# Kernel optimization log

Measured on AMD Instinct MI355X. Metric: run time of the kernel, lower is better.

Reference implementation:

```python
import jax, jax.numpy as jnp
import numpy as np

N, K, D, H, HD = 65536, 16, 96, 384, 256
DEPTH = 4

def _gelu(x):
    # torch nn.GELU default is exact erf-based
    return jax.nn.gelu(x, approximate=False)

def _bn(t, g, b):
    # eval-mode BatchNorm1d with running_mean=0, running_var=1 -> affine
    return t * g + b

def _mlp(f, w1, b1, w2, g, b):
    # Mlp: Linear(D,H)+GELU+Linear(H,D,no bias)+BN
    return _bn(_gelu(f @ w1 + b1) @ w2, g, b)


def setup_inputs() -> dict:
    key = jax.random.key(0)
    ks = jax.random.split(key, 32)
    def w(i, shape, s=0.05):
        return (jax.random.normal(ks[i], shape) * s).astype(jnp.float32)
    def g(i, shape):
        return (1.0 + 0.1 * jax.random.normal(ks[i], shape)).astype(jnp.float32)
    return dict(
        x=jax.random.normal(ks[0], (N, 4), jnp.float32),
        xyz=jax.random.uniform(ks[1], (N, 3), jnp.float32),
        knn=jax.random.randint(ks[2], (N, K), 0, N, dtype=jnp.int32),
        ne_w1=w(3, (7, 16)), ne_g1=g(4, (16,)), ne_b1=w(5, (16,)),
        ne_w2=w(6, (16, 32)), ne_g2=g(7, (32,)), ne_b2=w(8, (32,)),
        ne_w3=w(9, (32, D)),
        nbr_g=g(10, (D,)), nbr_b=w(11, (D,)),
        m0_w1=w(12, (D, H)), m0_b1=w(13, (H,)), m0_w2=w(14, (H, D)),
        m0_g=g(15, (D,)), m0_b=w(16, (D,)),
        lfp_w=w(17, (DEPTH, D, D)), lfp_g=g(18, (DEPTH, D)), lfp_b=w(19, (DEPTH, D)),
        ms_w1=w(20, (DEPTH // 2, D, H)), ms_b1=w(21, (DEPTH // 2, H)),
        ms_w2=w(22, (DEPTH // 2, H, D)), ms_g=g(23, (DEPTH // 2, D)), ms_b=w(24, (DEPTH // 2, D)),
        pp_g=g(25, (D,)), pp_b=w(26, (D,)), pp_w=w(27, (D, HD)),
    )


def reference(x, xyz, knn, ne_w1, ne_g1, ne_b1, ne_w2, ne_g2, ne_b2, ne_w3,
              nbr_g, nbr_b, m0_w1, m0_b1, m0_w2, m0_g, m0_b,
              lfp_w, lfp_g, lfp_b, ms_w1, ms_b1, ms_w2, ms_g, ms_b,
              pp_g, pp_b, pp_w):
    # --- neighbor embedding (first stage): rel-xyz + gathered raw features ---
    rel = xyz[knn] - xyz[:, None, :]               # [N,K,3]
    nbr = jnp.concatenate([rel, x[knn]], axis=-1)  # [N,K,7]
    h = _gelu(_bn(nbr @ ne_w1, ne_g1, ne_b1))      # [N,K,16]
    h = _gelu(_bn(h @ ne_w2, ne_g2, ne_b2))        # [N,K,32]
    h = h @ ne_w3                                  # [N,K,D]
    f = _bn(jnp.max(h, axis=1), nbr_g, nbr_b)      # edge max-pool -> [N,D]

    # --- Block: mlp + DEPTH x (LFP [+ Mlp every 2nd]) with residuals ---
    f = f + _mlp(f, m0_w1, m0_b1, m0_w2, m0_g, m0_b)
    for i in range(DEPTH):
        y = f @ lfp_w[i]                                       # proj [N,D]
        y = _bn(jnp.max(y[knn], axis=1) - y, lfp_g[i], lfp_b[i])  # knn edge maxpool
        f = f + y
        if i % 2 == 1:
            j = i // 2
            f = f + _mlp(f, ms_w1[j], ms_b1[j], ms_w2[j], ms_g[j], ms_b[j])

    # --- post projection head ---
    return _bn(f, pp_g, pp_b) @ pp_w               # [N,HD]
```

## Files before the change

kernel.cpp:

```cpp
#include <hip/hip_runtime.h>
#include <hip/hip_bf16.h>
#include <math.h>

#define NPTS 65536
#define KNB  16

typedef __attribute__((ext_vector_type(8))) short bf16x8;
typedef __attribute__((ext_vector_type(4))) float f32x4;

__device__ __forceinline__ float gelu_f(float v) {
    const float z  = v * 0.70710678118654752f;
    const float az = fabsf(z);
    const float t  = __builtin_amdgcn_rcpf(fmaf(0.3275911f, az, 1.0f));
    float p = fmaf(t, 1.061405429f, -1.453152027f);
    p = fmaf(t, p, 1.421413741f);
    p = fmaf(t, p, -0.284496736f);
    p = fmaf(t, p, 0.254829592f);
    p = p * t;
    const float e  = __expf(-z * z);
    float er = fmaf(-p, e, 1.0f);
    er = copysignf(er, z);
    return 0.5f * v * (1.0f + er);
}

__device__ __forceinline__ short f2bf_s(float v) {
    __hip_bfloat16 h = __float2bfloat16(v);
    return *reinterpret_cast<short*>(&h);
}

__global__ __launch_bounds__(256) void prep_weights(
    const float* __restrict__ m0_w1, const float* __restrict__ m0_w2,
    const float* __restrict__ ms_w1, const float* __restrict__ ms_w2,
    const float* __restrict__ lfp_w,
    const float* __restrict__ pp_w, const float* __restrict__ pp_g,
    const float* __restrict__ pp_b,
    __hip_bfloat16* __restrict__ w_m0w1t, __hip_bfloat16* __restrict__ w_m0w2t,
    __hip_bfloat16* __restrict__ w_msw1t, __hip_bfloat16* __restrict__ w_msw2t,
    __hip_bfloat16* __restrict__ w_lfpt,  __hip_bfloat16* __restrict__ w_ppt,
    float* __restrict__ c_pp)
{
    int idx = blockIdx.x * 256 + threadIdx.x;
    if (idx < 36864) {
        int n = idx / 96, k = idx % 96;
        w_m0w1t[idx] = __float2bfloat16(m0_w1[k * 384 + n]);
        return;
    }
    idx -= 36864;
    if (idx < 36864) {
        int n = idx / 384, k = idx % 384;
        w_m0w2t[idx] = __float2bfloat16(m0_w2[k * 96 + n]);
        return;
    }
    idx -= 36864;
    if (idx < 2 * 36864) {
        int j = idx / 36864, r = idx % 36864;
        int n = r / 96, k = r % 96;
        w_msw1t[idx] = __float2bfloat16(ms_w1[j * 36864 + k * 384 + n]);
        return;
    }
    idx -= 2 * 36864;
    if (idx < 2 * 36864) {
        int j = idx / 36864, r = idx % 36864;
        int n = r / 384, k = r % 384;
        w_msw2t[idx] = __float2bfloat16(ms_w2[j * 36864 + k * 96 + n]);
        return;
    }
    idx -= 2 * 36864;
    if (idx < 4 * 9216) {
        int i = idx / 9216, r = idx % 9216;
        int n = r / 96, k = r % 96;
        w_lfpt[idx] = __float2bfloat16(lfp_w[i * 9216 + k * 96 + n]);
        return;
    }
    idx -= 4 * 9216;
    if (idx < 24576) {
        int n = idx / 96, k = idx % 96;
        w_ppt[idx] = __float2bfloat16(pp_g[k] * pp_w[k * 256 + n]);
        return;
    }
    idx -= 24576;
    if (idx < 256) {
        float s = 0.f;
        for (int k = 0; k < 96; ++k) s += pp_b[k] * pp_w[k * 256 + idx];
        c_pp[idx] = s;
    }
}

__global__ __launch_bounds__(256) void ne_kernel(
    const float* __restrict__ x, const float* __restrict__ xyz,
    const int* __restrict__ knn,
    const float* __restrict__ w1, const float* __restrict__ g1, const float* __restrict__ b1,
    const float* __restrict__ w2, const float* __restrict__ g2, const float* __restrict__ b2,
    const float* __restrict__ w3,
    const float* __restrict__ ng, const float* __restrict__ nb,
    float* __restrict__ f, __hip_bfloat16* __restrict__ fbf)
{
    __shared__ float w1s[7 * 16];
    __shared__ float g1s[16], b1s[16], g2s[32], b2s[32];
    __shared__ float ngs[96], nbs[96];
    __shared__ short h16s[256][24];
    __shared__ short w2ts[32][40];
    __shared__ short h32s[256][40];
    __shared__ short w3t[96][40];

    const int tid = threadIdx.x;
    for (int i = tid; i < 112; i += 256) w1s[i] = w1[i];
    for (int i = tid; i < 1280; i += 256) {
        const int o = i / 40, kk = i % 40;
        w2ts[o][kk] = (kk < 16) ? f2bf_s(w2[kk * 32 + o]) : (short)0;
    }
    if (tid < 16) { g1s[tid] = g1[tid]; b1s[tid] = b1[tid]; }
    if (tid < 32) { g2s[tid] = g2[tid]; b2s[tid] = b2[tid]; }
    if (tid < 96) { ngs[tid] = ng[tid]; nbs[tid] = nb[tid]; }
    for (int i = tid; i < 3072; i += 256) {
        const int c = i / 96, n = i % 96;
        w3t[n][c] = f2bf_s(w3[i]);
    }
    __syncthreads();

    const int pl = tid >> 4;
    const int k  = tid & 15;
    const int p  = blockIdx.x * 16 + pl;
    const int j  = knn[p * KNB + k];

    float in7[7];
    {
        float cx0 = xyz[p * 3 + 0], cx1 = xyz[p * 3 + 1], cx2 = xyz[p * 3 + 2];
        in7[0] = xyz[j * 3 + 0] - cx0;
        in7[1] = xyz[j * 3 + 1] - cx1;
        in7[2] = xyz[j * 3 + 2] - cx2;
        in7[3] = x[j * 4 + 0];
        in7[4] = x[j * 4 + 1];
        in7[5] = x[j * 4 + 2];
        in7[6] = x[j * 4 + 3];
    }

    {
        bf16x8 t0, t1;
#pragma unroll
        for (int o = 0; o < 16; ++o) {
            float s = 0.f;
#pragma unroll
            for (int c = 0; c < 7; ++c) s += in7[c] * w1s[c * 16 + o];
            const float hv = gelu_f(s * g1s[o] + b1s[o]);
            if (o < 8) t0[o] = f2bf_s(hv); else t1[o - 8] = f2bf_s(hv);
        }
        *(bf16x8*)&h16s[tid][0] = t0;
        *(bf16x8*)&h16s[tid][8] = t1;
    }
    __syncthreads();

    const int wave = tid >> 6;
    const int lane = tid & 63;
    const int lr   = lane & 15;
    const int kc   = (lane >> 4) * 8;
    const f32x4 zero = {0.f, 0.f, 0.f, 0.f};
    const bf16x8 zero8 = {0, 0, 0, 0, 0, 0, 0, 0};

    {
        const float g2r0 = g2s[lr],      b2r0 = b2s[lr];
        const float g2r1 = g2s[16 + lr], b2r1 = b2s[16 + lr];
        const bf16x8 w2v0 = *(const bf16x8*)&w2ts[lr][kc];
        const bf16x8 w2v1 = *(const bf16x8*)&w2ts[16 + lr][kc];
#pragma unroll
        for (int pp = 0; pp < 4; ++pp) {
            const int lpl = wave * 4 + pp;
            bf16x8 av = zero8;
            if (lane < 32) av = *(const bf16x8*)&h16s[lpl * 16 + lr][kc];
            f32x4 c0 = __builtin_amdgcn_mfma_f32_16x16x32_bf16(av, w2v0, zero, 0, 0, 0);
            f32x4 c1 = __builtin_amdgcn_mfma_f32_16x16x32_bf16(av, w2v1, zero, 0, 0, 0);
#pragma unroll
            for (int r = 0; r < 4; ++r) {
                const int erow = lpl * 16 + (lane >> 4) * 4 + r;
                h32s[erow][lr]      = f2bf_s(gelu_f(fmaf(c0[r], g2r0, b2r0)));
                h32s[erow][16 + lr] = f2bf_s(gelu_f(fmaf(c1[r], g2r1, b2r1)));
            }
        }
    }
    __syncthreads();

    bf16x8 bv[6];
#pragma unroll
    for (int ct = 0; ct < 6; ++ct)
        bv[ct] = *(const bf16x8*)&w3t[ct * 16 + lr][kc];

#pragma unroll
    for (int pp = 0; pp < 4; ++pp) {
        const int lpl = wave * 4 + pp;
        const int gp  = blockIdx.x * 16 + lpl;
        const bf16x8 av = *(const bf16x8*)&h32s[lpl * 16 + lr][kc];
#pragma unroll
        for (int ct = 0; ct < 6; ++ct) {
            f32x4 a = __builtin_amdgcn_mfma_f32_16x16x32_bf16(av, bv[ct], zero, 0, 0, 0);
            float m = fmaxf(fmaxf(a[0], a[1]), fmaxf(a[2], a[3]));
            m = fmaxf(m, __shfl_xor(m, 16));
            m = fmaxf(m, __shfl_xor(m, 32));
            if (lane < 16) {
                const int d = ct * 16 + lane;
                const float val = m * ngs[d] + nbs[d];
                f[(size_t)gp * 96 + d] = val;
                fbf[(size_t)gp * 96 + d] = __float2bfloat16(val);
            }
        }
    }
}

__global__ __launch_bounds__(256) void mlp_fused(
    const __hip_bfloat16* __restrict__ w1t, const float* __restrict__ b1,
    const __hip_bfloat16* __restrict__ w2t,
    const float* __restrict__ g, const float* __restrict__ b,
    float* __restrict__ f, __hip_bfloat16* __restrict__ fbf)
{
    __shared__ short As[64 * 104];
    __shared__ short Hs[64 * 72];
    __shared__ short Bs[6912];
    __shared__ float bias_s[384];
    __shared__ float gs[96], bs[96];

    const int tid  = threadIdx.x;
    const int wave = tid >> 6;
    const int lane = tid & 63;
    const int lr   = lane & 15;
    const int kc   = (lane >> 4) * 8;
    const int row0 = blockIdx.x * 64;

    const short* fb = (const short*)fbf;
    const short* w1 = (const short*)w1t;
    const short* w2 = (const short*)w2t;

    {
        const int sr = tid >> 2, sk = (tid & 3) * 8;
#pragma unroll
        for (int i = 0; i < 3; ++i)
            *(bf16x8*)&As[sr * 104 + sk + 32 * i] =
                *(const bf16x8*)&fb[(size_t)(row0 + sr) * 96 + sk + 32 * i];
        for (int i = tid; i < 384; i += 256) bias_s[i] = b1[i];
        if (tid < 96) { gs[tid] = g[tid]; bs[tid] = b[tid]; }
    }

    f32x4 acc2[6];
#pragma unroll
    for (int i = 0; i < 6; ++i) acc2[i] = f32x4{0.f, 0.f, 0.f, 0.f};

    for (int c = 0; c < 6; ++c) {
        __syncthreads();
        {
            const int sr = tid >> 2, sk = (tid & 3) * 8;
#pragma unroll
            for (int i = 0; i < 3; ++i)
                *(bf16x8*)&Bs[sr * 104 + sk + 32 * i] =
                    *(const bf16x8*)&w1[(size_t)(c * 64 + sr) * 96 + sk + 32 * i];
        }
        __syncthreads();

        {
            f32x4 acc1[4];
#pragma unroll
            for (int i = 0; i < 4; ++i) acc1[i] = f32x4{0.f, 0.f, 0.f, 0.f};
#pragma unroll
            for (int k0 = 0; k0 < 96; k0 += 32) {
                const bf16x8 av = *(const bf16x8*)&As[(wave * 16 + lr) * 104 + k0 + kc];
#pragma unroll
                for (int ct = 0; ct < 4; ++ct) {
                    const bf16x8 bv = *(const bf16x8*)&Bs[(ct * 16 + lr) * 104 + k0 + kc];
                    acc1[ct] = __builtin_amdgcn_mfma_f32_16x16x32_bf16(av, bv, acc1[ct], 0, 0, 0);
                }
            }
            const int er = wave * 16 + ((lane >> 4) << 2);
#pragma unroll
            for (int ct = 0; ct < 4; ++ct) {
                const int cl = ct * 16 + lr;
                const float bb1 = bias_s[c * 64 + cl];
#pragma unroll
                for (int r = 0; r < 4; ++r)
                    Hs[(er + r) * 72 + cl] = f2bf_s(gelu_f(acc1[ct][r] + bb1));
            }
        }
        __syncthreads();

        {
            for (int i = tid; i < 768; i += 256) {
                const int r = i >> 3, ko = (i & 7) * 8;
                *(bf16x8*)&Bs[r * 72 + ko] =
                    *(const bf16x8*)&w2[(size_t)r * 384 + c * 64 + ko];
            }
        }
        __syncthreads();

#pragma unroll
        for (int ks = 0; ks < 64; ks += 32) {
            const bf16x8 av = *(const bf16x8*)&Hs[(wave * 16 + lr) * 72 + ks + kc];
#pragma unroll
            for (int ct = 0; ct < 6; ++ct) {
                const bf16x8 bv = *(const bf16x8*)&Bs[(ct * 16 + lr) * 72 + ks + kc];
                acc2[ct] = __builtin_amdgcn_mfma_f32_16x16x32_bf16(av, bv, acc2[ct], 0, 0, 0);
            }
        }
    }

    const int er = wave * 16 + ((lane >> 4) << 2);
#pragma unroll
    for (int ct = 0; ct < 6; ++ct) {
        const int col = ct * 16 + lr;
        const float gg = gs[col], bb = bs[col];
#pragma unroll
        for (int r = 0; r < 4; ++r) {
            const size_t o = (size_t)(row0 + er + r) * 96 + col;
            const float nf = f[o] + acc2[ct][r] * gg + bb;
            f[o] = nf;
            fbf[o] = __float2bfloat16(nf);
        }
    }
}

__global__ __launch_bounds__(256) void proj_kernel(
    const __hip_bfloat16* __restrict__ fbf,
    const __hip_bfloat16* __restrict__ wT,
    float* __restrict__ y)
{
    __shared__ short As[64 * 104];
    __shared__ short Ws[96 * 104];

    const int tid  = threadIdx.x;
    const int wave = tid >> 6;
    const int lane = tid & 63;
    const int lr   = lane & 15;
    const int kc   = (lane >> 4) * 8;
    const int row0 = blockIdx.x * 64;

    const short* fb = (const short*)fbf;
    const short* wg = (const short*)wT;

    {
        const int sr = tid >> 2, sk = (tid & 3) * 8;
#pragma unroll
        for (int i = 0; i < 3; ++i)
            *(bf16x8*)&As[sr * 104 + sk + 32 * i] =
                *(const bf16x8*)&fb[(size_t)(row0 + sr) * 96 + sk + 32 * i];
        for (int i = tid; i < 1152; i += 256) {
            const int r = i / 12, ko = (i % 12) * 8;
            *(bf16x8*)&Ws[r * 104 + ko] = *(const bf16x8*)&wg[(size_t)r * 96 + ko];
        }
    }
    __syncthreads();

    f32x4 acc[6];
#pragma unroll
    for (int i = 0; i < 6; ++i) acc[i] = f32x4{0.f, 0.f, 0.f, 0.f};

#pragma unroll
    for (int k0 = 0; k0 < 96; k0 += 32) {
        const bf16x8 av = *(const bf16x8*)&As[(wave * 16 + lr) * 104 + k0 + kc];
#pragma unroll
        for (int ct = 0; ct < 6; ++ct) {
            const bf16x8 bv = *(const bf16x8*)&Ws[(ct * 16 + lr) * 104 + k0 + kc];
            acc[ct] = __builtin_amdgcn_mfma_f32_16x16x32_bf16(av, bv, acc[ct], 0, 0, 0);
        }
    }

    const int er = wave * 16 + ((lane >> 4) << 2);
#pragma unroll
    for (int ct = 0; ct < 6; ++ct) {
        const int col = ct * 16 + lr;
#pragma unroll
        for (int r = 0; r < 4; ++r)
            y[(size_t)(row0 + er + r) * 96 + col] = acc[ct][r];
    }
}

__global__ __launch_bounds__(256) void head_kernel(
    const __hip_bfloat16* __restrict__ fbf,
    const __hip_bfloat16* __restrict__ wT,
    const float* __restrict__ c_pp,
    float* __restrict__ out)
{
    __shared__ short As[64 * 104];
    __shared__ short Bs[64 * 104];
    __shared__ float cpps[256];

    const int tid  = threadIdx.x;
    const int wave = tid >> 6;
    const int lane = tid & 63;
    const int lr   = lane & 15;
    const int kc   = (lane >> 4) * 8;
    const int row0 = blockIdx.x * 64;

    const short* fb = (const short*)fbf;
    const short* wg = (const short*)wT;

    {
        const int sr = tid >> 2, sk = (tid & 3) * 8;
#pragma unroll
        for (int i = 0; i < 3; ++i)
            *(bf16x8*)&As[sr * 104 + sk + 32 * i] =
                *(const bf16x8*)&fb[(size_t)(row0 + sr) * 96 + sk + 32 * i];
        if (tid < 256) cpps[tid] = c_pp[tid];
    }

    for (int nt = 0; nt < 4; ++nt) {
        __syncthreads();
        {
            const int sr = tid >> 2, sk = (tid & 3) * 8;
#pragma unroll
            for (int i = 0; i < 3; ++i)
                *(bf16x8*)&Bs[sr * 104 + sk + 32 * i] =
                    *(const bf16x8*)&wg[(size_t)(nt * 64 + sr) * 96 + sk + 32 * i];
        }
        __syncthreads();

        f32x4 acc[4];
#pragma unroll
        for (int i = 0; i < 4; ++i) acc[i] = f32x4{0.f, 0.f, 0.f, 0.f};
#pragma unroll
        for (int k0 = 0; k0 < 96; k0 += 32) {
            const bf16x8 av = *(const bf16x8*)&As[(wave * 16 + lr) * 104 + k0 + kc];
#pragma unroll
            for (int ct = 0; ct < 4; ++ct) {
                const bf16x8 bv = *(const bf16x8*)&Bs[(ct * 16 + lr) * 104 + k0 + kc];
                acc[ct] = __builtin_amdgcn_mfma_f32_16x16x32_bf16(av, bv, acc[ct], 0, 0, 0);
            }
        }

        const int er = wave * 16 + ((lane >> 4) << 2);
#pragma unroll
        for (int ct = 0; ct < 4; ++ct) {
            const int col = nt * 64 + ct * 16 + lr;
#pragma unroll
            for (int r = 0; r < 4; ++r)
                out[(size_t)(row0 + er + r) * 256 + col] = acc[ct][r] + cpps[col];
        }
    }
}

__global__ __launch_bounds__(256) void gathermax_kernel(
    const float* __restrict__ y, const int* __restrict__ knn,
    const float* __restrict__ g, const float* __restrict__ b,
    float* __restrict__ f, __hip_bfloat16* __restrict__ fbf)
{
    __shared__ int knns[16][16];
    const int tid = threadIdx.x;
    const int pl  = tid >> 4;
    const int t   = tid & 15;
    const int p0  = blockIdx.x * 16;
    knns[pl][t] = knn[(p0 + pl) * KNB + t];
    __syncthreads();

    const int p   = p0 + pl;
    const int off = t * 6;

    float m[6];
#pragma unroll
    for (int i = 0; i < 6; ++i) m[i] = -INFINITY;

#pragma unroll 4
    for (int k = 0; k < 16; ++k) {
        const int j = knns[pl][k];
        const float* yr = y + (size_t)j * 96 + off;
        const float2 v0 = *(const float2*)(yr + 0);
        const float2 v1 = *(const float2*)(yr + 2);
        const float2 v2 = *(const float2*)(yr + 4);
        m[0] = fmaxf(m[0], v0.x); m[1] = fmaxf(m[1], v0.y);
        m[2] = fmaxf(m[2], v1.x); m[3] = fmaxf(m[3], v1.y);
        m[4] = fmaxf(m[4], v2.x); m[5] = fmaxf(m[5], v2.y);
    }

    const float* yc = y + (size_t)p * 96 + off;
    float* fr = f + (size_t)p * 96 + off;
    __hip_bfloat16* fbr = fbf + (size_t)p * 96 + off;
#pragma unroll
    for (int i = 0; i < 6; ++i) {
        const float nf = fr[i] + (m[i] - yc[i]) * g[off + i] + b[off + i];
        fr[i] = nf;
        fbr[i] = __float2bfloat16(nf);
    }
}

extern "C" void kernel_launch(void* const* d_in, const int* in_sizes, int n_in,
                              void* d_out, int out_size, void* d_ws, size_t ws_size,
                              hipStream_t stream)
{
    const float* x     = (const float*)d_in[0];
    const float* xyz   = (const float*)d_in[1];
    const int*   knn   = (const int*)d_in[2];
    const float* ne_w1 = (const float*)d_in[3];
    const float* ne_g1 = (const float*)d_in[4];
    const float* ne_b1 = (const float*)d_in[5];
    const float* ne_w2 = (const float*)d_in[6];
    const float* ne_g2 = (const float*)d_in[7];
    const float* ne_b2 = (const float*)d_in[8];
    const float* ne_w3 = (const float*)d_in[9];
    const float* nbr_g = (const float*)d_in[10];
    const float* nbr_b = (const float*)d_in[11];
    const float* m0_w1 = (const float*)d_in[12];
    const float* m0_b1 = (const float*)d_in[13];
    const float* m0_w2 = (const float*)d_in[14];
    const float* m0_g  = (const float*)d_in[15];
    const float* m0_b  = (const float*)d_in[16];
    const float* lfp_w = (const float*)d_in[17];
    const float* lfp_g = (const float*)d_in[18];
    const float* lfp_b = (const float*)d_in[19];
    const float* ms_w1 = (const float*)d_in[20];
    const float* ms_b1 = (const float*)d_in[21];
    const float* ms_w2 = (const float*)d_in[22];
    const float* ms_g  = (const float*)d_in[23];
    const float* ms_b  = (const float*)d_in[24];
    const float* pp_g  = (const float*)d_in[25];
    const float* pp_b  = (const float*)d_in[26];
    const float* pp_w  = (const float*)d_in[27];

    float* out = (float*)d_out;

    float* f   = (float*)d_ws;
    float* y   = f + (size_t)NPTS * 96;
    __hip_bfloat16* fbf = (__hip_bfloat16*)(y + (size_t)NPTS * 96);
    __hip_bfloat16* w_m0w1t = fbf + (size_t)NPTS * 96;
    __hip_bfloat16* w_m0w2t = w_m0w1t + 36864;
    __hip_bfloat16* w_msw1t = w_m0w2t + 36864;
    __hip_bfloat16* w_msw2t = w_msw1t + 2 * 36864;
    __hip_bfloat16* w_lfpt  = w_msw2t + 2 * 36864;
    __hip_bfloat16* w_ppt   = w_lfpt + 4 * 9216;
    float* c_pp = (float*)(w_ppt + 24576);

    prep_weights<<<1105, 256, 0, stream>>>(
        m0_w1, m0_w2, ms_w1, ms_w2, lfp_w, pp_w, pp_g, pp_b,
        w_m0w1t, w_m0w2t, w_msw1t, w_msw2t, w_lfpt, w_ppt, c_pp);

    ne_kernel<<<NPTS / 16, 256, 0, stream>>>(x, xyz, knn,
        ne_w1, ne_g1, ne_b1, ne_w2, ne_g2, ne_b2, ne_w3, nbr_g, nbr_b, f, fbf);

    mlp_fused<<<NPTS / 64, 256, 0, stream>>>(
        w_m0w1t, m0_b1, w_m0w2t, m0_g, m0_b, f, fbf);

    for (int i = 0; i < 4; ++i) {
        proj_kernel<<<NPTS / 64, 256, 0, stream>>>(
            fbf, w_lfpt + (size_t)i * 9216, y);
        gathermax_kernel<<<NPTS / 16, 256, 0, stream>>>(
            y, knn, lfp_g + i * 96, lfp_b + i * 96, f, fbf);
        if (i & 1) {
            const int jj = i / 2;
            mlp_fused<<<NPTS / 64, 256, 0, stream>>>(
                w_msw1t + (size_t)jj * 36864, ms_b1 + (size_t)jj * 384,
                w_msw2t + (size_t)jj * 36864, ms_g + jj * 96, ms_b + jj * 96, f, fbf);
        }
    }

    head_kernel<<<NPTS / 64, 256, 0, stream>>>(fbf, w_ppt, c_pp, out);
}
```

Measured before the change: 600.3 us.

## Amortize weight staging over more points per block in embedding, MLP and projection

The neighbor-embedding kernel now handles 64 points per block by looping over four 16-point groups. The w2/w3 bf16 fragments and the BN scales are loaded once into registers straight from global memory, replacing the shared-memory transposes that each block redid. The fused MLP and LFP projection kernels now process 128 rows per block, with each wave covering two 16-row tiles, so each staged weight tile is reused over twice as many rows. The cost is fewer blocks, more accumulator registers and larger LDS use, which may lower occupancy.

```diff
diff --git a/kernel.cpp b/kernel.cpp
--- a/kernel.cpp
+++ b/kernel.cpp
@@ -95,73 +95,85 @@
     const float* __restrict__ ng, const float* __restrict__ nb,
     float* __restrict__ f, __hip_bfloat16* __restrict__ fbf)
 {
-    __shared__ float w1s[7 * 16];
-    __shared__ float g1s[16], b1s[16], g2s[32], b2s[32];
-    __shared__ float ngs[96], nbs[96];
+    __shared__ float w1s[112];
+    __shared__ float g1s[16], b1s[16];
     __shared__ short h16s[256][24];
-    __shared__ short w2ts[32][40];
     __shared__ short h32s[256][40];
-    __shared__ short w3t[96][40];
-
-    const int tid = threadIdx.x;
-    for (int i = tid; i < 112; i += 256) w1s[i] = w1[i];
-    for (int i = tid; i < 1280; i += 256) {
-        const int o = i / 40, kk = i % 40;
-        w2ts[o][kk] = (kk < 16) ? f2bf_s(w2[kk * 32 + o]) : (short)0;
-    }
-    if (tid < 16) { g1s[tid] = g1[tid]; b1s[tid] = b1[tid]; }
-    if (tid < 32) { g2s[tid] = g2[tid]; b2s[tid] = b2[tid]; }
-    if (tid < 96) { ngs[tid] = ng[tid]; nbs[tid] = nb[tid]; }
-    for (int i = tid; i < 3072; i += 256) {
-        const int c = i / 96, n = i % 96;
-        w3t[n][c] = f2bf_s(w3[i]);
-    }
-    __syncthreads();
-
-    const int pl = tid >> 4;
-    const int k  = tid & 15;
-    const int p  = blockIdx.x * 16 + pl;
-    const int j  = knn[p * KNB + k];
-
-    float in7[7];
-    {
-        float cx0 = xyz[p * 3 + 0], cx1 = xyz[p * 3 + 1], cx2 = xyz[p * 3 + 2];
-        in7[0] = xyz[j * 3 + 0] - cx0;
-        in7[1] = xyz[j * 3 + 1] - cx1;
-        in7[2] = xyz[j * 3 + 2] - cx2;
-        in7[3] = x[j * 4 + 0];
-        in7[4] = x[j * 4 + 1];
-        in7[5] = x[j * 4 + 2];
-        in7[6] = x[j * 4 + 3];
-    }
-
-    {
-        bf16x8 t0, t1;
-#pragma unroll
-        for (int o = 0; o < 16; ++o) {
-            float s = 0.f;
-#pragma unroll
-            for (int c = 0; c < 7; ++c) s += in7[c] * w1s[c * 16 + o];
-            const float hv = gelu_f(s * g1s[o] + b1s[o]);
-            if (o < 8) t0[o] = f2bf_s(hv); else t1[o - 8] = f2bf_s(hv);
-        }
-        *(bf16x8*)&h16s[tid][0] = t0;
-        *(bf16x8*)&h16s[tid][8] = t1;
-    }
-    __syncthreads();
-
+
+    const int tid  = threadIdx.x;
     const int wave = tid >> 6;
     const int lane = tid & 63;
     const int lr   = lane & 15;
     const int kc   = (lane >> 4) * 8;
+
+    if (tid < 112) w1s[tid] = w1[tid];
+    if (tid < 16) { g1s[tid] = g1[tid]; b1s[tid] = b1[tid]; }
+
     const f32x4 zero = {0.f, 0.f, 0.f, 0.f};
     const bf16x8 zero8 = {0, 0, 0, 0, 0, 0, 0, 0};
 
-    {
-        const float g2r0 = g2s[lr],      b2r0 = b2s[lr];
-        const float g2r1 = g2s[16 + lr], b2r1 = b2s[16 + lr];
-        const bf16x8 w2v0 = *(const bf16x8*)&w2ts[lr][kc];
-        const bf16x8 w2v1 = *(const bf16x8*)&w2ts[16 + lr][kc];
+    bf16x8 w2v0 = zero8, w2v1 = zero8;
+    if (lane < 32) {
+#pragma unroll
+        for (int j = 0; j < 8; ++j) {
+            w2v0[j] = f2bf_s(w2[(kc + j) * 32 + lr]);
+            w2v1[j] = f2bf_s(w2[(kc + j) * 32 + 16 + lr]);
+        }
+    }
+    bf16x8 bv[6];
+#pragma unroll
+    for (int ct = 0; ct < 6; ++ct)
+#pragma unroll
+        for (int j = 0; j < 8; ++j)
+            bv[ct][j] = f2bf_s(w3[(kc + j) * 96 + ct * 16 + lr]);
+
+    const float g2r0 = g2[lr],      b2r0 = b2[lr];
+    const float g2r1 = g2[16 + lr], b2r1 = b2[16 + lr];
+    float ngv[6], nbv[6];
+    if (lane < 16) {
+#pragma unroll
+        for (int ct = 0; ct < 6; ++ct) {
+            ngv[ct] = ng[ct * 16 + lane];
+            nbv[ct] = nb[ct * 16 + lane];
+        }
+    }
+
+    const int pl = tid >> 4;
+    const int k  = tid & 15;
+    __syncthreads();
+
+#pragma unroll 1
+    for (int grp = 0; grp < 4; ++grp) {
+        const int p = blockIdx.x * 64 + grp * 16 + pl;
+        const int j = knn[p * KNB + k];
+
+        float in7[7];
+        {
+            float cx0 = xyz[p * 3 + 0], cx1 = xyz[p * 3 + 1], cx2 = xyz[p * 3 + 2];
+            in7[0] = xyz[j * 3 + 0] - cx0;
+            in7[1] = xyz[j * 3 + 1] - cx1;
+            in7[2] = xyz[j * 3 + 2] - cx2;
+            in7[3] = x[j * 4 + 0];
+            in7[4] = x[j * 4 + 1];
+            in7[5] = x[j * 4 + 2];
+            in7[6] = x[j * 4 + 3];
+        }
+
+        {
+            bf16x8 t0, t1;
+#pragma unroll
+            for (int o = 0; o < 16; ++o) {
+                float s = 0.f;
+#pragma unroll
+                for (int c = 0; c < 7; ++c) s += in7[c] * w1s[c * 16 + o];
+                const float hv = gelu_f(s * g1s[o] + b1s[o]);
+                if (o < 8) t0[o] = f2bf_s(hv); else t1[o - 8] = f2bf_s(hv);
+            }
+            *(bf16x8*)&h16s[tid][0] = t0;
+            *(bf16x8*)&h16s[tid][8] = t1;
+        }
+        __syncthreads();
+
 #pragma unroll
         for (int pp = 0; pp < 4; ++pp) {
             const int lpl = wave * 4 + pp;
@@ -176,30 +188,24 @@
                 h32s[erow][16 + lr] = f2bf_s(gelu_f(fmaf(c1[r], g2r1, b2r1)));
             }
         }
-    }
-    __syncthreads();
-
-    bf16x8 bv[6];
-#pragma unroll
-    for (int ct = 0; ct < 6; ++ct)
-        bv[ct] = *(const bf16x8*)&w3t[ct * 16 + lr][kc];
-
-#pragma unroll
-    for (int pp = 0; pp < 4; ++pp) {
-        const int lpl = wave * 4 + pp;
-        const int gp  = blockIdx.x * 16 + lpl;
-        const bf16x8 av = *(const bf16x8*)&h32s[lpl * 16 + lr][kc];
-#pragma unroll
-        for (int ct = 0; ct < 6; ++ct) {
-            f32x4 a = __builtin_amdgcn_mfma_f32_16x16x32_bf16(av, bv[ct], zero, 0, 0, 0);
-            float m = fmaxf(fmaxf(a[0], a[1]), fmaxf(a[2], a[3]));
-            m = fmaxf(m, __shfl_xor(m, 16));
-            m = fmaxf(m, __shfl_xor(m, 32));
-            if (lane < 16) {
-                const int d = ct * 16 + lane;
-                const float val = m * ngs[d] + nbs[d];
-                f[(size_t)gp * 96 + d] = val;
-                fbf[(size_t)gp * 96 + d] = __float2bfloat16(val);
+        __syncthreads();
+
+#pragma unroll
+        for (int pp = 0; pp < 4; ++pp) {
+            const int lpl = wave * 4 + pp;
+            const int gp  = blockIdx.x * 64 + grp * 16 + lpl;
+            const bf16x8 av = *(const bf16x8*)&h32s[lpl * 16 + lr][kc];
+#pragma unroll
+            for (int ct = 0; ct < 6; ++ct) {
+                f32x4 a = __builtin_amdgcn_mfma_f32_16x16x32_bf16(av, bv[ct], zero, 0, 0, 0);
+                float m = fmaxf(fmaxf(a[0], a[1]), fmaxf(a[2], a[3]));
+                m = fmaxf(m, __shfl_xor(m, 16));
+                m = fmaxf(m, __shfl_xor(m, 32));
+                if (lane < 16) {
+                    const float val = m * ngv[ct] + nbv[ct];
+                    f[(size_t)gp * 96 + ct * 16 + lane] = val;
+                    fbf[(size_t)gp * 96 + ct * 16 + lane] = __float2bfloat16(val);
+                }
             }
         }
     }
@@ -211,11 +217,193 @@
     const float* __restrict__ g, const float* __restrict__ b,
     float* __restrict__ f, __hip_bfloat16* __restrict__ fbf)
 {
-    __shared__ short As[64 * 104];
-    __shared__ short Hs[64 * 72];
-    __shared__ short Bs[6912];
+    __shared__ short As[128 * 104];
+    __shared__ short Hs[128 * 72];
+    __shared__ short Bs[96 * 72];
     __shared__ float bias_s[384];
     __shared__ float gs[96], bs[96];
+
+    const int tid  = threadIdx.x;
+    const int wave = tid >> 6;
+    const int lane = tid & 63;
+    const int lr   = lane & 15;
+    const int kc   = (lane >> 4) * 8;
+    const int row0 = blockIdx.x * 128;
+
+    const short* fb = (const short*)fbf;
+    const short* w1 = (const short*)w1t;
+    const short* w2 = (const short*)w2t;
+
+    for (int i = tid; i < 128 * 12; i += 256) {
+        const int r = i / 12, c8 = (i % 12) * 8;
+        *(bf16x8*)&As[r * 104 + c8] = *(const bf16x8*)&fb[(size_t)(row0 + r) * 96 + c8];
+    }
+    for (int i = tid; i < 384; i += 256) bias_s[i] = b1[i];
+    if (tid < 96) { gs[tid] = g[tid]; bs[tid] = b[tid]; }
+
+    f32x4 acc2[2][6];
+#pragma unroll
+    for (int rt = 0; rt < 2; ++rt)
+#pragma unroll
+        for (int i = 0; i < 6; ++i) acc2[rt][i] = f32x4{0.f, 0.f, 0.f, 0.f};
+
+    for (int c = 0; c < 6; ++c) {
+        __syncthreads();
+        for (int i = tid; i < 64 * 12; i += 256) {
+            const int r = i / 12, c8 = (i % 12) * 8;
+            *(bf16x8*)&Bs[r * 104 + c8] =
+                *(const bf16x8*)&w1[(size_t)(c * 64 + r) * 96 + c8];
+        }
+        __syncthreads();
+
+        {
+            f32x4 acc1[2][4];
+#pragma unroll
+            for (int rt = 0; rt < 2; ++rt)
+#pragma unroll
+                for (int i = 0; i < 4; ++i) acc1[rt][i] = f32x4{0.f, 0.f, 0.f, 0.f};
+#pragma unroll
+            for (int k0 = 0; k0 < 96; k0 += 32) {
+#pragma unroll
+                for (int rt = 0; rt < 2; ++rt) {
+                    const bf16x8 av =
+                        *(const bf16x8*)&As[((wave * 2 + rt) * 16 + lr) * 104 + k0 + kc];
+#pragma unroll
+                    for (int ct = 0; ct < 4; ++ct) {
+                        const bf16x8 bvv =
+                            *(const bf16x8*)&Bs[(ct * 16 + lr) * 104 + k0 + kc];
+                        acc1[rt][ct] =
+                            __builtin_amdgcn_mfma_f32_16x16x32_bf16(av, bvv, acc1[rt][ct], 0, 0, 0);
+                    }
+                }
+            }
+#pragma unroll
+            for (int rt = 0; rt < 2; ++rt) {
+                const int er = (wave * 2 + rt) * 16 + ((lane >> 4) << 2);
+#pragma unroll
+                for (int ct = 0; ct < 4; ++ct) {
+                    const int cl = ct * 16 + lr;
+                    const float bb1 = bias_s[c * 64 + cl];
+#pragma unroll
+                    for (int r = 0; r < 4; ++r)
+                        Hs[(er + r) * 72 + cl] = f2bf_s(gelu_f(acc1[rt][ct][r] + bb1));
+                }
+            }
+        }
+        __syncthreads();
+
+        for (int i = tid; i < 96 * 8; i += 256) {
+            const int r = i >> 3, ko = (i & 7) * 8;
+            *(bf16x8*)&Bs[r * 72 + ko] =
+                *(const bf16x8*)&w2[(size_t)r * 384 + c * 64 + ko];
+        }
+        __syncthreads();
+
+#pragma unroll
+        for (int ks = 0; ks < 64; ks += 32) {
+#pragma unroll
+            for (int rt = 0; rt < 2; ++rt) {
+                const bf16x8 av =
+                    *(const bf16x8*)&Hs[((wave * 2 + rt) * 16 + lr) * 72 + ks + kc];
+#pragma unroll
+                for (int ct = 0; ct < 6; ++ct) {
+                    const bf16x8 bvv = *(const bf16x8*)&Bs[(ct * 16 + lr) * 72 + ks + kc];
+                    acc2[rt][ct] =
+                        __builtin_amdgcn_mfma_f32_16x16x32_bf16(av, bvv, acc2[rt][ct], 0, 0, 0);
+                }
+            }
+        }
+    }
+
+#pragma unroll
+    for (int rt = 0; rt < 2; ++rt) {
+        const int er = (wave * 2 + rt) * 16 + ((lane >> 4) << 2);
+#pragma unroll
+        for (int ct = 0; ct < 6; ++ct) {
+            const int col = ct * 16 + lr;
+            const float gg = gs[col], bb = bs[col];
+#pragma unroll
+            for (int r = 0; r < 4; ++r) {
+                const size_t o = (size_t)(row0 + er + r) * 96 + col;
+                const float nf = f[o] + acc2[rt][ct][r] * gg + bb;
+                f[o] = nf;
+                fbf[o] = __float2bfloat16(nf);
+            }
+        }
+    }
+}
+
+__global__ __launch_bounds__(256) void proj_kernel(
+    const __hip_bfloat16* __restrict__ fbf,
+    const __hip_bfloat16* __restrict__ wT,
+    float* __restrict__ y)
+{
+    __shared__ short As[128 * 104];
+    __shared__ short Ws[96 * 104];
+
+    const int tid  = threadIdx.x;
+    const int wave = tid >> 6;
+    const int lane = tid & 63;
+    const int lr   = lane & 15;
+    const int kc   = (lane >> 4) * 8;
+    const int row0 = blockIdx.x * 128;
+
+    const short* fb = (const short*)fbf;
+    const short* wg = (const short*)wT;
+
+    for (int i = tid; i < 128 * 12; i += 256) {
+        const int r = i / 12, c8 = (i % 12) * 8;
+        *(bf16x8*)&As[r * 104 + c8] = *(const bf16x8*)&fb[(size_t)(row0 + r) * 96 + c8];
+    }
+    for (int i = tid; i < 96 * 12; i += 256) {
+        const int r = i / 12, c8 = (i % 12) * 8;
+        *(bf16x8*)&Ws[r * 104 + c8] = *(const bf16x8*)&wg[(size_t)r * 96 + c8];
+    }
+    __syncthreads();
+
+    f32x4 acc[2][6];
+#pragma unroll
+    for (int rt = 0; rt < 2; ++rt)
+#pragma unroll
+        for (int i = 0; i < 6; ++i) acc[rt][i] = f32x4{0.f, 0.f, 0.f, 0.f};
+
+#pragma unroll
+    for (int k0 = 0; k0 < 96; k0 += 32) {
+#pragma unroll
+        for (int rt = 0; rt < 2; ++rt) {
+            const bf16x8 av =
+                *(const bf16x8*)&As[((wave * 2 + rt) * 16 + lr) * 104 + k0 + kc];
+#pragma unroll
+            for (int ct = 0; ct < 6; ++ct) {
+                const bf16x8 bvv = *(const bf16x8*)&Ws[(ct * 16 + lr) * 104 + k0 + kc];
+                acc[rt][ct] =
+                    __builtin_amdgcn_mfma_f32_16x16x32_bf16(av, bvv, acc[rt][ct], 0, 0, 0);
+            }
+        }
+    }
+
+#pragma unroll
+    for (int rt = 0; rt < 2; ++rt) {
+        const int er = (wave * 2 + rt) * 16 + ((lane >> 4) << 2);
+#pragma unroll
+        for (int ct = 0; ct < 6; ++ct) {
+            const int col = ct * 16 + lr;
+#pragma unroll
+            for (int r = 0; r < 4; ++r)
+                y[(size_t)(row0 + er + r) * 96 + col] = acc[rt][ct][r];
+        }
+    }
+}
+
+__global__ __launch_bounds__(256) void head_kernel(
+    const __hip_bfloat16* __restrict__ fbf,
+    const __hip_bfloat16* __restrict__ wT,
+    const float* __restrict__ c_pp,
+    float* __restrict__ out)
+{
+    __shared__ short As[64 * 104];
+    __shared__ short Bs[64 * 104];
+    __shared__ float cpps[256];
 
     const int tid  = threadIdx.x;
     const int wave = tid >> 6;
@@ -225,167 +413,6 @@
     const int row0 = blockIdx.x * 64;
 
     const short* fb = (const short*)fbf;
-    const short* w1 = (const short*)w1t;
-    const short* w2 = (const short*)w2t;
-
-    {
-        const int sr = tid >> 2, sk = (tid & 3) * 8;
-#pragma unroll
-        for (int i = 0; i < 3; ++i)
-            *(bf16x8*)&As[sr * 104 + sk + 32 * i] =
-                *(const bf16x8*)&fb[(size_t)(row0 + sr) * 96 + sk + 32 * i];
-        for (int i = tid; i < 384; i += 256) bias_s[i] = b1[i];
-        if (tid < 96) { gs[tid] = g[tid]; bs[tid] = b[tid]; }
-    }
-
-    f32x4 acc2[6];
-#pragma unroll
-    for (int i = 0; i < 6; ++i) acc2[i] = f32x4{0.f, 0.f, 0.f, 0.f};
-
-    for (int c = 0; c < 6; ++c) {
-        __syncthreads();
-        {
-            const int sr = tid >> 2, sk = (tid & 3) * 8;
-#pragma unroll
-            for (int i = 0; i < 3; ++i)
-                *(bf16x8*)&Bs[sr * 104 + sk + 32 * i] =
-                    *(const bf16x8*)&w1[(size_t)(c * 64 + sr) * 96 + sk + 32 * i];
-        }
-        __syncthreads();
-
-        {
-            f32x4 acc1[4];
-#pragma unroll
-            for (int i = 0; i < 4; ++i) acc1[i] = f32x4{0.f, 0.f, 0.f, 0.f};
-#pragma unroll
-            for (int k0 = 0; k0 < 96; k0 += 32) {
-                const bf16x8 av = *(const bf16x8*)&As[(wave * 16 + lr) * 104 + k0 + kc];
-#pragma unroll
-                for (int ct = 0; ct < 4; ++ct) {
-                    const bf16x8 bv = *(const bf16x8*)&Bs[(ct * 16 + lr) * 104 + k0 + kc];
-                    acc1[ct] = __builtin_amdgcn_mfma_f32_16x16x32_bf16(av, bv, acc1[ct], 0, 0, 0);
-                }
-            }
-            const int er = wave * 16 + ((lane >> 4) << 2);
-#pragma unroll
-            for (int ct = 0; ct < 4; ++ct) {
-                const int cl = ct * 16 + lr;
-                const float bb1 = bias_s[c * 64 + cl];
-#pragma unroll
-                for (int r = 0; r < 4; ++r)
-                    Hs[(er + r) * 72 + cl] = f2bf_s(gelu_f(acc1[ct][r] + bb1));
-            }
-        }
-        __syncthreads();
-
-        {
-            for (int i = tid; i < 768; i += 256) {
-                const int r = i >> 3, ko = (i & 7) * 8;
-                *(bf16x8*)&Bs[r * 72 + ko] =
-                    *(const bf16x8*)&w2[(size_t)r * 384 + c * 64 + ko];
-            }
-        }
-        __syncthreads();
-
-#pragma unroll
-        for (int ks = 0; ks < 64; ks += 32) {
-            const bf16x8 av = *(const bf16x8*)&Hs[(wave * 16 + lr) * 72 + ks + kc];
-#pragma unroll
-            for (int ct = 0; ct < 6; ++ct) {
-                const bf16x8 bv = *(const bf16x8*)&Bs[(ct * 16 + lr) * 72 + ks + kc];
-                acc2[ct] = __builtin_amdgcn_mfma_f32_16x16x32_bf16(av, bv, acc2[ct], 0, 0, 0);
-            }
-        }
-    }
-
-    const int er = wave * 16 + ((lane >> 4) << 2);
-#pragma unroll
-    for (int ct = 0; ct < 6; ++ct) {
-        const int col = ct * 16 + lr;
-        const float gg = gs[col], bb = bs[col];
-#pragma unroll
-        for (int r = 0; r < 4; ++r) {
-            const size_t o = (size_t)(row0 + er + r) * 96 + col;
-            const float nf = f[o] + acc2[ct][r] * gg + bb;
-            f[o] = nf;
-            fbf[o] = __float2bfloat16(nf);
-        }
-    }
-}
-
-__global__ __launch_bounds__(256) void proj_kernel(
-    const __hip_bfloat16* __restrict__ fbf,
-    const __hip_bfloat16* __restrict__ wT,
-    float* __restrict__ y)
-{
-    __shared__ short As[64 * 104];
-    __shared__ short Ws[96 * 104];
-
-    const int tid  = threadIdx.x;
-    const int wave = tid >> 6;
-    const int lane = tid & 63;
-    const int lr   = lane & 15;
-    const int kc   = (lane >> 4) * 8;
-    const int row0 = blockIdx.x * 64;
-
-    const short* fb = (const short*)fbf;
-    const short* wg = (const short*)wT;
-
-    {
-        const int sr = tid >> 2, sk = (tid & 3) * 8;
-#pragma unroll
-        for (int i = 0; i < 3; ++i)
-            *(bf16x8*)&As[sr * 104 + sk + 32 * i] =
-                *(const bf16x8*)&fb[(size_t)(row0 + sr) * 96 + sk + 32 * i];
-        for (int i = tid; i < 1152; i += 256) {
-            const int r = i / 12, ko = (i % 12) * 8;
-            *(bf16x8*)&Ws[r * 104 + ko] = *(const bf16x8*)&wg[(size_t)r * 96 + ko];
-        }
-    }
-    __syncthreads();
-
-    f32x4 acc[6];
-#pragma unroll
-    for (int i = 0; i < 6; ++i) acc[i] = f32x4{0.f, 0.f, 0.f, 0.f};
-
-#pragma unroll
-    for (int k0 = 0; k0 < 96; k0 += 32) {
-        const bf16x8 av = *(const bf16x8*)&As[(wave * 16 + lr) * 104 + k0 + kc];
-#pragma unroll
-        for (int ct = 0; ct < 6; ++ct) {
-            const bf16x8 bv = *(const bf16x8*)&Ws[(ct * 16 + lr) * 104 + k0 + kc];
-            acc[ct] = __builtin_amdgcn_mfma_f32_16x16x32_bf16(av, bv, acc[ct], 0, 0, 0);
-        }
-    }
-
-    const int er = wave * 16 + ((lane >> 4) << 2);
-#pragma unroll
-    for (int ct = 0; ct < 6; ++ct) {
-        const int col = ct * 16 + lr;
-#pragma unroll
-        for (int r = 0; r < 4; ++r)
-            y[(size_t)(row0 + er + r) * 96 + col] = acc[ct][r];
-    }
-}
-
-__global__ __launch_bounds__(256) void head_kernel(
-    const __hip_bfloat16* __restrict__ fbf,
-    const __hip_bfloat16* __restrict__ wT,
-    const float* __restrict__ c_pp,
-    float* __restrict__ out)
-{
-    __shared__ short As[64 * 104];
-    __shared__ short Bs[64 * 104];
-    __shared__ float cpps[256];
-
-    const int tid  = threadIdx.x;
-    const int wave = tid >> 6;
-    const int lane = tid & 63;
-    const int lr   = lane & 15;
-    const int kc   = (lane >> 4) * 8;
-    const int row0 = blockIdx.x * 64;
-
-    const short* fb = (const short*)fbf;
     const short* wg = (const short*)wT;
 
     {
@@ -416,8 +443,8 @@
             const bf16x8 av = *(const bf16x8*)&As[(wave * 16 + lr) * 104 + k0 + kc];
 #pragma unroll
             for (int ct = 0; ct < 4; ++ct) {
-                const bf16x8 bv = *(const bf16x8*)&Bs[(ct * 16 + lr) * 104 + k0 + kc];
-                acc[ct] = __builtin_amdgcn_mfma_f32_16x16x32_bf16(av, bv, acc[ct], 0, 0, 0);
+                const bf16x8 bvv = *(const bf16x8*)&Bs[(ct * 16 + lr) * 104 + k0 + kc];
+                acc[ct] = __builtin_amdgcn_mfma_f32_16x16x32_bf16(av, bvv, acc[ct], 0, 0, 0);
             }
         }
 
@@ -525,20 +552,20 @@
         m0_w1, m0_w2, ms_w1, ms_w2, lfp_w, pp_w, pp_g, pp_b,
         w_m0w1t, w_m0w2t, w_msw1t, w_msw2t, w_lfpt, w_ppt, c_pp);
 
-    ne_kernel<<<NPTS / 16, 256, 0, stream>>>(x, xyz, knn,
+    ne_kernel<<<NPTS / 64, 256, 0, stream>>>(x, xyz, knn,
         ne_w1, ne_g1, ne_b1, ne_w2, ne_g2, ne_b2, ne_w3, nbr_g, nbr_b, f, fbf);
 
-    mlp_fused<<<NPTS / 64, 256, 0, stream>>>(
+    mlp_fused<<<NPTS / 128, 256, 0, stream>>>(
         w_m0w1t, m0_b1, w_m0w2t, m0_g, m0_b, f, fbf);
 
     for (int i = 0; i < 4; ++i) {
-        proj_kernel<<<NPTS / 64, 256, 0, stream>>>(
+        proj_kernel<<<NPTS / 128, 256, 0, stream>>>(
             fbf, w_lfpt + (size_t)i * 9216, y);
         gathermax_kernel<<<NPTS / 16, 256, 0, stream>>>(
             y, knn, lfp_g + i * 96, lfp_b + i * 96, f, fbf);
         if (i & 1) {
             const int jj = i / 2;
-            mlp_fused<<<NPTS / 64, 256, 0, stream>>>(
+            mlp_fused<<<NPTS / 128, 256, 0, stream>>>(
                 w_msw1t + (size_t)jj * 36864, ms_b1 + (size_t)jj * 384,
                 w_msw2t + (size_t)jj * 36864, ms_g + jj * 96, ms_b + jj * 96, f, fbf);
         }
```

Result: slower. 615.6 us (+2.5%).

## Store LFP projections as fp16 and amortize neighbor-embedding weight setup over 64 points

Applied to the files above, without the earlier changes.

The projection output y is now written as fp16 and read back as half2 in the knn gather-max kernel. This halves the bytes of the random-access gather traffic and of the projection stores, at some precision cost in the max-pool input. The neighbor-embedding kernel now loops over four 16-point groups per block, and the w2/w3 weights and BN parameters are loaded straight into registers instead of being transposed into shared memory. This removes the repeated per-block weight staging, at the cost of higher register use and one-quarter as many blocks.

```diff
diff --git a/kernel.cpp b/kernel.cpp
--- a/kernel.cpp
+++ b/kernel.cpp
@@ -1,5 +1,6 @@
 #include <hip/hip_runtime.h>
 #include <hip/hip_bf16.h>
+#include <hip/hip_fp16.h>
 #include <math.h>
 
 #define NPTS 65536
@@ -95,73 +96,85 @@
     const float* __restrict__ ng, const float* __restrict__ nb,
     float* __restrict__ f, __hip_bfloat16* __restrict__ fbf)
 {
-    __shared__ float w1s[7 * 16];
-    __shared__ float g1s[16], b1s[16], g2s[32], b2s[32];
-    __shared__ float ngs[96], nbs[96];
+    __shared__ float w1s[112];
+    __shared__ float g1s[16], b1s[16];
     __shared__ short h16s[256][24];
-    __shared__ short w2ts[32][40];
     __shared__ short h32s[256][40];
-    __shared__ short w3t[96][40];
-
-    const int tid = threadIdx.x;
-    for (int i = tid; i < 112; i += 256) w1s[i] = w1[i];
-    for (int i = tid; i < 1280; i += 256) {
-        const int o = i / 40, kk = i % 40;
-        w2ts[o][kk] = (kk < 16) ? f2bf_s(w2[kk * 32 + o]) : (short)0;
-    }
-    if (tid < 16) { g1s[tid] = g1[tid]; b1s[tid] = b1[tid]; }
-    if (tid < 32) { g2s[tid] = g2[tid]; b2s[tid] = b2[tid]; }
-    if (tid < 96) { ngs[tid] = ng[tid]; nbs[tid] = nb[tid]; }
-    for (int i = tid; i < 3072; i += 256) {
-        const int c = i / 96, n = i % 96;
-        w3t[n][c] = f2bf_s(w3[i]);
-    }
-    __syncthreads();
-
-    const int pl = tid >> 4;
-    const int k  = tid & 15;
-    const int p  = blockIdx.x * 16 + pl;
-    const int j  = knn[p * KNB + k];
-
-    float in7[7];
-    {
-        float cx0 = xyz[p * 3 + 0], cx1 = xyz[p * 3 + 1], cx2 = xyz[p * 3 + 2];
-        in7[0] = xyz[j * 3 + 0] - cx0;
-        in7[1] = xyz[j * 3 + 1] - cx1;
-        in7[2] = xyz[j * 3 + 2] - cx2;
-        in7[3] = x[j * 4 + 0];
-        in7[4] = x[j * 4 + 1];
-        in7[5] = x[j * 4 + 2];
-        in7[6] = x[j * 4 + 3];
-    }
-
-    {
-        bf16x8 t0, t1;
-#pragma unroll
-        for (int o = 0; o < 16; ++o) {
-            float s = 0.f;
-#pragma unroll
-            for (int c = 0; c < 7; ++c) s += in7[c] * w1s[c * 16 + o];
-            const float hv = gelu_f(s * g1s[o] + b1s[o]);
-            if (o < 8) t0[o] = f2bf_s(hv); else t1[o - 8] = f2bf_s(hv);
-        }
-        *(bf16x8*)&h16s[tid][0] = t0;
-        *(bf16x8*)&h16s[tid][8] = t1;
-    }
-    __syncthreads();
-
+
+    const int tid  = threadIdx.x;
     const int wave = tid >> 6;
     const int lane = tid & 63;
     const int lr   = lane & 15;
     const int kc   = (lane >> 4) * 8;
+
+    if (tid < 112) w1s[tid] = w1[tid];
+    if (tid < 16) { g1s[tid] = g1[tid]; b1s[tid] = b1[tid]; }
+
     const f32x4 zero = {0.f, 0.f, 0.f, 0.f};
     const bf16x8 zero8 = {0, 0, 0, 0, 0, 0, 0, 0};
 
-    {
-        const float g2r0 = g2s[lr],      b2r0 = b2s[lr];
-        const float g2r1 = g2s[16 + lr], b2r1 = b2s[16 + lr];
-        const bf16x8 w2v0 = *(const bf16x8*)&w2ts[lr][kc];
-        const bf16x8 w2v1 = *(const bf16x8*)&w2ts[16 + lr][kc];
+    bf16x8 w2v0 = zero8, w2v1 = zero8;
+    if (lane < 32) {
+#pragma unroll
+        for (int j = 0; j < 8; ++j) {
+            w2v0[j] = f2bf_s(w2[(kc + j) * 32 + lr]);
+            w2v1[j] = f2bf_s(w2[(kc + j) * 32 + 16 + lr]);
+        }
+    }
+    bf16x8 bv[6];
+#pragma unroll
+    for (int ct = 0; ct < 6; ++ct)
+#pragma unroll
+        for (int j = 0; j < 8; ++j)
+            bv[ct][j] = f2bf_s(w3[(kc + j) * 96 + ct * 16 + lr]);
+
+    const float g2r0 = g2[lr],      b2r0 = b2[lr];
+    const float g2r1 = g2[16 + lr], b2r1 = b2[16 + lr];
+    float ngv[6], nbv[6];
+    if (lane < 16) {
+#pragma unroll
+        for (int ct = 0; ct < 6; ++ct) {
+            ngv[ct] = ng[ct * 16 + lane];
+            nbv[ct] = nb[ct * 16 + lane];
+        }
+    }
+
+    const int pl = tid >> 4;
+    const int k  = tid & 15;
+    __syncthreads();
+
+#pragma unroll 1
+    for (int grp = 0; grp < 4; ++grp) {
+        const int p = blockIdx.x * 64 + grp * 16 + pl;
+        const int j = knn[p * KNB + k];
+
+        float in7[7];
+        {
+            float cx0 = xyz[p * 3 + 0], cx1 = xyz[p * 3 + 1], cx2 = xyz[p * 3 + 2];
+            in7[0] = xyz[j * 3 + 0] - cx0;
+            in7[1] = xyz[j * 3 + 1] - cx1;
+            in7[2] = xyz[j * 3 + 2] - cx2;
+            in7[3] = x[j * 4 + 0];
+            in7[4] = x[j * 4 + 1];
+            in7[5] = x[j * 4 + 2];
+            in7[6] = x[j * 4 + 3];
+        }
+
+        {
+            bf16x8 t0, t1;
+#pragma unroll
+            for (int o = 0; o < 16; ++o) {
+                float s = 0.f;
+#pragma unroll
+                for (int c = 0; c < 7; ++c) s += in7[c] * w1s[c * 16 + o];
+                const float hv = gelu_f(s * g1s[o] + b1s[o]);
+                if (o < 8) t0[o] = f2bf_s(hv); else t1[o - 8] = f2bf_s(hv);
+            }
+            *(bf16x8*)&h16s[tid][0] = t0;
+            *(bf16x8*)&h16s[tid][8] = t1;
+        }
+        __syncthreads();
+
 #pragma unroll
         for (int pp = 0; pp < 4; ++pp) {
             const int lpl = wave * 4 + pp;
@@ -176,30 +189,24 @@
                 h32s[erow][16 + lr] = f2bf_s(gelu_f(fmaf(c1[r], g2r1, b2r1)));
             }
         }
-    }
-    __syncthreads();
-
-    bf16x8 bv[6];
-#pragma unroll
-    for (int ct = 0; ct < 6; ++ct)
-        bv[ct] = *(const bf16x8*)&w3t[ct * 16 + lr][kc];
-
-#pragma unroll
-    for (int pp = 0; pp < 4; ++pp) {
-        const int lpl = wave * 4 + pp;
-        const int gp  = blockIdx.x * 16 + lpl;
-        const bf16x8 av = *(const bf16x8*)&h32s[lpl * 16 + lr][kc];
-#pragma unroll
-        for (int ct = 0; ct < 6; ++ct) {
-            f32x4 a = __builtin_amdgcn_mfma_f32_16x16x32_bf16(av, bv[ct], zero, 0, 0, 0);
-            float m = fmaxf(fmaxf(a[0], a[1]), fmaxf(a[2], a[3]));
-            m = fmaxf(m, __shfl_xor(m, 16));
-            m = fmaxf(m, __shfl_xor(m, 32));
-            if (lane < 16) {
-                const int d = ct * 16 + lane;
-                const float val = m * ngs[d] + nbs[d];
-                f[(size_t)gp * 96 + d] = val;
-                fbf[(size_t)gp * 96 + d] = __float2bfloat16(val);
+        __syncthreads();
+
+#pragma unroll
+        for (int pp = 0; pp < 4; ++pp) {
+            const int lpl = wave * 4 + pp;
+            const int gp  = blockIdx.x * 64 + grp * 16 + lpl;
+            const bf16x8 av = *(const bf16x8*)&h32s[lpl * 16 + lr][kc];
+#pragma unroll
+            for (int ct = 0; ct < 6; ++ct) {
+                f32x4 a = __builtin_amdgcn_mfma_f32_16x16x32_bf16(av, bv[ct], zero, 0, 0, 0);
+                float m = fmaxf(fmaxf(a[0], a[1]), fmaxf(a[2], a[3]));
+                m = fmaxf(m, __shfl_xor(m, 16));
+                m = fmaxf(m, __shfl_xor(m, 32));
+                if (lane < 16) {
+                    const float val = m * ngv[ct] + nbv[ct];
+                    f[(size_t)gp * 96 + ct * 16 + lane] = val;
+                    fbf[(size_t)gp * 96 + ct * 16 + lane] = __float2bfloat16(val);
+                }
             }
         }
     }
@@ -262,8 +269,8 @@
                 const bf16x8 av = *(const bf16x8*)&As[(wave * 16 + lr) * 104 + k0 + kc];
 #pragma unroll
                 for (int ct = 0; ct < 4; ++ct) {
-                    const bf16x8 bv = *(const bf16x8*)&Bs[(ct * 16 + lr) * 104 + k0 + kc];
-                    acc1[ct] = __builtin_amdgcn_mfma_f32_16x16x32_bf16(av, bv, acc1[ct], 0, 0, 0);
+                    const bf16x8 bvv = *(const bf16x8*)&Bs[(ct * 16 + lr) * 104 + k0 + kc];
+                    acc1[ct] = __builtin_amdgcn_mfma_f32_16x16x32_bf16(av, bvv, acc1[ct], 0, 0, 0);
                 }
             }
             const int er = wave * 16 + ((lane >> 4) << 2);
@@ -292,8 +299,8 @@
             const bf16x8 av = *(const bf16x8*)&Hs[(wave * 16 + lr) * 72 + ks + kc];
 #pragma unroll
             for (int ct = 0; ct < 6; ++ct) {
-                const bf16x8 bv = *(const bf16x8*)&Bs[(ct * 16 + lr) * 72 + ks + kc];
-                acc2[ct] = __builtin_amdgcn_mfma_f32_16x16x32_bf16(av, bv, acc2[ct], 0, 0, 0);
+                const bf16x8 bvv = *(const bf16x8*)&Bs[(ct * 16 + lr) * 72 + ks + kc];
+                acc2[ct] = __builtin_amdgcn_mfma_f32_16x16x32_bf16(av, bvv, acc2[ct], 0, 0, 0);
             }
         }
     }
@@ -316,7 +323,7 @@
 __global__ __launch_bounds__(256) void proj_kernel(
     const __hip_bfloat16* __restrict__ fbf,
     const __hip_bfloat16* __restrict__ wT,
-    float* __restrict__ y)
+    __half* __restrict__ y)
 {
     __shared__ short As[64 * 104];
     __shared__ short Ws[96 * 104];
@@ -353,8 +360,8 @@
         const bf16x8 av = *(const bf16x8*)&As[(wave * 16 + lr) * 104 + k0 + kc];
 #pragma unroll
         for (int ct = 0; ct < 6; ++ct) {
-            const bf16x8 bv = *(const bf16x8*)&Ws[(ct * 16 + lr) * 104 + k0 + kc];
-            acc[ct] = __builtin_amdgcn_mfma_f32_16x16x32_bf16(av, bv, acc[ct], 0, 0, 0);
+            const bf16x8 bvv = *(const bf16x8*)&Ws[(ct * 16 + lr) * 104 + k0 + kc];
+            acc[ct] = __builtin_amdgcn_mfma_f32_16x16x32_bf16(av, bvv, acc[ct], 0, 0, 0);
         }
     }
 
@@ -364,7 +371,7 @@
         const int col = ct * 16 + lr;
 #pragma unroll
         for (int r = 0; r < 4; ++r)
-            y[(size_t)(row0 + er + r) * 96 + col] = acc[ct][r];
+            y[(size_t)(row0 + er + r) * 96 + col] = __float2half(acc[ct][r]);
     }
 }
 
@@ -416,8 +423,8 @@
             const bf16x8 av = *(const bf16x8*)&As[(wave * 16 + lr) * 104 + k0 + kc];
 #pragma unroll
             for (int ct = 0; ct < 4; ++ct) {
-                const bf16x8 bv = *(const bf16x8*)&Bs[(ct * 16 + lr) * 104 + k0 + kc];
-                acc[ct] = __builtin_amdgcn_mfma_f32_16x16x32_bf16(av, bv, acc[ct], 0, 0, 0);
+                const bf16x8 bvv = *(const bf16x8*)&Bs[(ct * 16 + lr) * 104 + k0 + kc];
+                acc[ct] = __builtin_amdgcn_mfma_f32_16x16x32_bf16(av, bvv, acc[ct], 0, 0, 0);
             }
         }
 
@@ -433,7 +440,7 @@
 }
 
 __global__ __launch_bounds__(256) void gathermax_kernel(
-    const float* __restrict__ y, const int* __restrict__ knn,
+    const __half* __restrict__ y, const int* __restrict__ knn,
     const float* __restrict__ g, const float* __restrict__ b,
     float* __restrict__ f, __hip_bfloat16* __restrict__ fbf)
 {
@@ -455,21 +462,26 @@
 #pragma unroll 4
     for (int k = 0; k < 16; ++k) {
         const int j = knns[pl][k];
-        const float* yr = y + (size_t)j * 96 + off;
-        const float2 v0 = *(const float2*)(yr + 0);
-        const float2 v1 = *(const float2*)(yr + 2);
-        const float2 v2 = *(const float2*)(yr + 4);
+        const __half* yr = y + (size_t)j * 96 + off;
+        const float2 v0 = __half22float2(*(const __half2*)(yr + 0));
+        const float2 v1 = __half22float2(*(const __half2*)(yr + 2));
+        const float2 v2 = __half22float2(*(const __half2*)(yr + 4));
         m[0] = fmaxf(m[0], v0.x); m[1] = fmaxf(m[1], v0.y);
         m[2] = fmaxf(m[2], v1.x); m[3] = fmaxf(m[3], v1.y);
         m[4] = fmaxf(m[4], v2.x); m[5] = fmaxf(m[5], v2.y);
     }
 
-    const float* yc = y + (size_t)p * 96 + off;
+    const __half* yc = y + (size_t)p * 96 + off;
+    const float2 c0 = __half22float2(*(const __half2*)(yc + 0));
+    const float2 c1 = __half22float2(*(const __half2*)(yc + 2));
+    const float2 c2 = __half22float2(*(const __half2*)(yc + 4));
+    const float cself[6] = {c0.x, c0.y, c1.x, c1.y, c2.x, c2.y};
+
     float* fr = f + (size_t)p * 96 + off;
     __hip_bfloat16* fbr = fbf + (size_t)p * 96 + off;
 #pragma unroll
     for (int i = 0; i < 6; ++i) {
-        const float nf = fr[i] + (m[i] - yc[i]) * g[off + i] + b[off + i];
+        const float nf = fr[i] + (m[i] - cself[i]) * g[off + i] + b[off + i];
         fr[i] = nf;
         fbr[i] = __float2bfloat16(nf);
     }
@@ -511,8 +523,8 @@
     float* out = (float*)d_out;
 
     float* f   = (float*)d_ws;
-    float* y   = f + (size_t)NPTS * 96;
-    __hip_bfloat16* fbf = (__hip_bfloat16*)(y + (size_t)NPTS * 96);
+    __half* y  = (__half*)(f + (size_t)NPTS * 96);
+    __hip_bfloat16* fbf = (__hip_bfloat16*)((float*)y + (size_t)NPTS * 96);
     __hip_bfloat16* w_m0w1t = fbf + (size_t)NPTS * 96;
     __hip_bfloat16* w_m0w2t = w_m0w1t + 36864;
     __hip_bfloat16* w_msw1t = w_m0w2t + 36864;
@@ -525,7 +537,7 @@
         m0_w1, m0_w2, ms_w1, ms_w2, lfp_w, pp_w, pp_g, pp_b,
         w_m0w1t, w_m0w2t, w_msw1t, w_msw2t, w_lfpt, w_ppt, c_pp);
 
-    ne_kernel<<<NPTS / 16, 256, 0, stream>>>(x, xyz, knn,
+    ne_kernel<<<NPTS / 64, 256, 0, stream>>>(x, xyz, knn,
         ne_w1, ne_g1, ne_b1, ne_w2, ne_g2, ne_b2, ne_w3, nbr_g, nbr_b, f, fbf);
 
     mlp_fused<<<NPTS / 64, 256, 0, stream>>>(
```

New measurement: 493.0 us. -17.9%, faster.
